# Kernel tuning notes

Measured on AMD Instinct MI355X. Metric: run time of the kernel, lower is better.

Reference implementation:

```python
import jax, jax.numpy as jnp
import numpy as np

B, S, H, E, D, K = 2, 2048, 2048, 8, 2048, 2


def setup_inputs() -> dict:
    key = jax.random.key(0)
    ks = jax.random.split(key, 4)
    # lecun_normal-style scaling: std = 1/sqrt(fan_in)
    return {
        "x": jax.random.normal(ks[0], (B, S, H), jnp.float32),
        "router_w": jax.random.normal(ks[1], (H, E), jnp.float32) / np.sqrt(H).astype(np.float32),
        "router_b": jnp.zeros((E,), jnp.float32),
        "expert_w": jax.random.normal(ks[2], (E, H, D), jnp.float32) / np.sqrt(H).astype(np.float32),
        "expert_b": jnp.zeros((E, D), jnp.float32),
        "out_w": jax.random.normal(ks[3], (D, D), jnp.float32) / np.sqrt(D).astype(np.float32),
        "out_b": jnp.zeros((D,), jnp.float32),
    }


def reference(x, router_w, router_b, expert_w, expert_b, out_w, out_b):
    num_experts = expert_w.shape[0]
    # Router: logits -> softmax -> top-2 -> renormalize
    router_logits = jnp.einsum("bsh,he->bse", x, router_w) + router_b
    router_probs = jax.nn.softmax(router_logits, axis=-1)
    top_k_probs, top_k_indices = jax.lax.top_k(router_probs, K)  # [B,S,K]
    top_k_probs = top_k_probs / jnp.sum(top_k_probs, axis=-1, keepdims=True)
    # Per-expert gate weight: sum of top-k probs routed to that expert. [B,S,E]
    onehot = jax.nn.one_hot(top_k_indices, num_experts, dtype=x.dtype)  # [B,S,K,E]
    gates = jnp.einsum("bsk,bske->bse", top_k_probs, onehot)
    # Dense per-expert GEMM + gelu (mask-and-multiply MoE; gate==0 kills unrouted tokens)
    expert_out = jax.nn.gelu(jnp.einsum("bsh,ehd->ebsd", x, expert_w) + expert_b[:, None, None, :])
    combined = jnp.einsum("bse,ebsd->bsd", gates, expert_out)
    # Output projection
    return jnp.einsum("bsd,df->bsf", combined, out_w) + out_b
```

## Files before the change

### kernel.cpp

```cpp
#include <hip/hip_runtime.h>
#include <stdint.h>

#define H_DIM 2048
#define E_NUM 8
#define D_DIM 2048
#define NTOK 4096
#define BM 128
#define BN 128
#define BK 32

typedef __bf16 bf16x8 __attribute__((ext_vector_type(8)));
typedef float f32x4 __attribute__((ext_vector_type(4)));

__device__ __forceinline__ unsigned short f2bf(float f) {
    union { float f; uint32_t u; } c; c.f = f;
    uint32_t r = (c.u + 0x7FFFu + ((c.u >> 16) & 1u)) >> 16;
    return (unsigned short)r;
}
__device__ __forceinline__ float bf2f(unsigned short h) {
    union { float f; uint32_t u; } c; c.u = ((uint32_t)h) << 16;
    return c.f;
}

__device__ __forceinline__ void gl_lds16(const unsigned short* g, unsigned short* l) {
    __builtin_amdgcn_global_load_lds(
        (const __attribute__((address_space(1))) unsigned int*)g,
        (__attribute__((address_space(3))) unsigned int*)l, 16, 0, 0);
}

__global__ __launch_bounds__(256) void router_cvt_kernel(
    const float* __restrict__ x, const float* __restrict__ rw,
    const float* __restrict__ rb, int* __restrict__ counts,
    uint32_t* __restrict__ tok, float* __restrict__ gate,
    unsigned short* __restrict__ xb) {
    int t = (blockIdx.x * 256 + threadIdx.x) >> 6;
    int lane = threadIdx.x & 63;
    const float* xr = x + (size_t)t * H_DIM;
    unsigned short* xo = xb + (size_t)t * H_DIM;
    float p[E_NUM];
#pragma unroll
    for (int e = 0; e < E_NUM; e++) p[e] = 0.f;
#pragma unroll
    for (int pass = 0; pass < H_DIM / 256; pass++) {
        int h = pass * 256 + lane * 4;
        float4 v = *(const float4*)(xr + h);
        ushort4 o;
        o.x = f2bf(v.x); o.y = f2bf(v.y); o.z = f2bf(v.z); o.w = f2bf(v.w);
        *(ushort4*)(xo + h) = o;
        const float* r0 = rw + (size_t)h * E_NUM;
#pragma unroll
        for (int e = 0; e < E_NUM; e++)
            p[e] += v.x * r0[e] + v.y * r0[e + 8] + v.z * r0[e + 16] + v.w * r0[e + 24];
    }
#pragma unroll
    for (int e = 0; e < E_NUM; e++) {
#pragma unroll
        for (int off = 1; off < 64; off <<= 1) p[e] += __shfl_xor(p[e], off, 64);
    }
    if (lane == 0) {
        float l[E_NUM];
#pragma unroll
        for (int e = 0; e < E_NUM; e++) l[e] = p[e] + rb[e];
        int e0 = 0;
#pragma unroll
        for (int e = 1; e < E_NUM; e++) if (l[e] > l[e0]) e0 = e;
        int e1 = (e0 == 0) ? 1 : 0;
#pragma unroll
        for (int e = 0; e < E_NUM; e++) if (e != e0 && l[e] > l[e1]) e1 = e;
        float g0 = 1.f / (1.f + __expf(l[e1] - l[e0]));
        float g1 = 1.f - g0;
        int p0 = atomicAdd(&counts[e0], 1);
        tok[e0 * NTOK + p0] = (uint32_t)t;
        gate[e0 * NTOK + p0] = g0;
        int p1 = atomicAdd(&counts[e1], 1);
        tok[e1 * NTOK + p1] = (uint32_t)t | (1u << 16);
        gate[e1 * NTOK + p1] = g1;
    }
}

__global__ __launch_bounds__(256) void transpose_cvt_kernel(
    const float* __restrict__ ew, const float* __restrict__ ow,
    unsigned short* __restrict__ ewT) {
    __shared__ unsigned short t[64][136];
    int z = blockIdx.z;
    const float* s = (z < 8) ? (ew + (size_t)z * H_DIM * D_DIM) : ow;
    unsigned short* d = ewT + (size_t)z * H_DIM * D_DIM;
    int n0 = blockIdx.x * 64, k0 = blockIdx.y * 128;
    int tid = threadIdx.x;
    int rr = tid >> 4;
    int c4 = (tid & 15) * 4;
#pragma unroll
    for (int p = 0; p < 8; p++) {
        int k = p * 16 + rr;
        float4 v = *(const float4*)(s + (size_t)(k0 + k) * D_DIM + n0 + c4);
        t[c4 + 0][k] = f2bf(v.x);
        t[c4 + 1][k] = f2bf(v.y);
        t[c4 + 2][k] = f2bf(v.z);
        t[c4 + 3][k] = f2bf(v.w);
    }
    __syncthreads();
    int kc = (tid & 15) * 8;
#pragma unroll
    for (int p = 0; p < 4; p++) {
        int n = p * 16 + rr;
        uint4 v = *(const uint4*)&t[n][kc];
        *(uint4*)(d + (size_t)(n0 + n) * H_DIM + k0 + kc) = v;
    }
}

__global__ __launch_bounds__(256) void expert_gemm_kernel(
    const unsigned short* __restrict__ xb,
    const unsigned short* __restrict__ ewT,
    const float* __restrict__ eb,
    const int* __restrict__ counts,
    const uint32_t* __restrict__ tok,
    const float* __restrict__ gate,
    unsigned short* __restrict__ Y)
{
    int e = blockIdx.z;
    int cnt = counts[e];
    int m0 = blockIdx.y * BM;
    if (m0 >= cnt) return;
    int n0 = blockIdx.x * BN;

    __shared__ unsigned short As[BM][BK];
    __shared__ unsigned short Bs[BN][BK];
    __shared__ uint32_t tok_s[BM];
    __shared__ float gate_s[BM];

    int tid = threadIdx.x;
    if (tid < BM) {
        int idx = m0 + tid;
        uint32_t tk = 0; float g = 0.f;
        if (idx < cnt) { tk = tok[e * NTOK + idx]; g = gate[e * NTOK + idx]; }
        tok_s[tid] = tk; gate_s[tid] = g;
    }
    __syncthreads();

    int lane = tid & 63;
    int wave = tid >> 6;
    int sr = lane >> 2;
    int sc = ((lane & 3) ^ ((lane >> 3) & 3)) * 8;
    int r0 = wave * 32 + sr;
    int r1 = wave * 32 + 16 + sr;
    const unsigned short* agp0 = xb + (size_t)(tok_s[r0] & 0xFFFFu) * H_DIM + sc;
    const unsigned short* agp1 = xb + (size_t)(tok_s[r1] & 0xFFFFu) * H_DIM + sc;
    const unsigned short* bbase = ewT + (size_t)e * D_DIM * H_DIM;
    const unsigned short* bgp0 = bbase + (size_t)(n0 + r0) * H_DIM + sc;
    const unsigned short* bgp1 = bbase + (size_t)(n0 + r1) * H_DIM + sc;
    unsigned short* la0 = &As[wave * 32][0];
    unsigned short* la1 = &As[wave * 32 + 16][0];
    unsigned short* lb0 = &Bs[wave * 32][0];
    unsigned short* lb1 = &Bs[wave * 32 + 16][0];

    int wm = (wave >> 1) * 64;
    int wn = (wave & 1) * 64;
    int row16 = lane & 15;
    int quad = lane >> 4;
    int slot = (quad ^ ((row16 >> 1) & 3)) * 16;
    int aoffA[4], aoffB[4];
#pragma unroll
    for (int i = 0; i < 4; i++) {
        aoffA[i] = (wm + i * 16 + row16) * (BK * 2) + slot;
        aoffB[i] = (wn + i * 16 + row16) * (BK * 2) + slot;
    }
    const char* pA = (const char*)&As[0][0];
    const char* pB = (const char*)&Bs[0][0];

    f32x4 acc[4][4];
#pragma unroll
    for (int i = 0; i < 4; i++)
#pragma unroll
        for (int j = 0; j < 4; j++) acc[i][j] = (f32x4)(0.f);

    for (int kk = 0; kk < H_DIM; kk += BK) {
        __syncthreads();
        gl_lds16(agp0 + kk, la0);
        gl_lds16(agp1 + kk, la1);
        gl_lds16(bgp0 + kk, lb0);
        gl_lds16(bgp1 + kk, lb1);
        __syncthreads();
        bf16x8 af[4], bff[4];
#pragma unroll
        for (int i = 0; i < 4; i++) {
            af[i] = *(const bf16x8*)(pA + aoffA[i]);
            bff[i] = *(const bf16x8*)(pB + aoffB[i]);
        }
#pragma unroll
        for (int i = 0; i < 4; i++)
#pragma unroll
            for (int j = 0; j < 4; j++)
                acc[i][j] = __builtin_amdgcn_mfma_f32_16x16x32_bf16(
                    af[i], bff[j], acc[i][j], 0, 0, 0);
    }

#pragma unroll
    for (int i = 0; i < 4; i++) {
        int rbase = wm + i * 16 + quad * 4;
#pragma unroll
        for (int j = 0; j < 4; j++) {
            int n = n0 + wn + j * 16 + row16;
            float bias = eb[e * D_DIM + n];
#pragma unroll
            for (int r = 0; r < 4; r++) {
                int lrow = rbase + r;
                if (m0 + lrow < cnt) {
                    uint32_t tk = tok_s[lrow];
                    float g = gate_s[lrow];
                    float v = acc[i][j][r] + bias;
                    float q = 0.7978845608028654f * (v + 0.044715f * v * v * v);
                    float gl = v / (1.f + __expf(-2.f * q));
                    int token = tk & 0xFFFF;
                    int slot2 = (tk >> 16) & 1;
                    Y[((size_t)token * 2 + slot2) * D_DIM + n] = f2bf(g * gl);
                }
            }
        }
    }
}

__global__ __launch_bounds__(256) void combine_kernel(
    const unsigned short* __restrict__ Y, unsigned short* __restrict__ comb) {
    int i = blockIdx.x * 256 + threadIdx.x;
    int t = i >> 8;
    int dc = (i & 255) * 8;
    uint4 u0 = *(const uint4*)(Y + (size_t)t * 2 * D_DIM + dc);
    uint4 u1 = *(const uint4*)(Y + ((size_t)t * 2 + 1) * D_DIM + dc);
    uint4 o;
    uint32_t* po = (uint32_t*)&o;
    const uint32_t* p0 = (const uint32_t*)&u0;
    const uint32_t* p1 = (const uint32_t*)&u1;
#pragma unroll
    for (int k = 0; k < 4; k++) {
        uint32_t a = p0[k], b = p1[k];
        float s0 = bf2f((unsigned short)(a & 0xFFFF)) + bf2f((unsigned short)(b & 0xFFFF));
        float s1 = bf2f((unsigned short)(a >> 16)) + bf2f((unsigned short)(b >> 16));
        po[k] = (uint32_t)f2bf(s0) | ((uint32_t)f2bf(s1) << 16);
    }
    *(uint4*)(comb + (size_t)t * D_DIM + dc) = o;
}

__global__ __launch_bounds__(256) void out_gemm_kernel(
    const unsigned short* __restrict__ comb,
    const unsigned short* __restrict__ owT,
    const float* __restrict__ ob,
    float* __restrict__ out) {
    int m0 = blockIdx.y * BM, n0 = blockIdx.x * BN;
    __shared__ unsigned short As[BM][BK];
    __shared__ unsigned short Bs[BN][BK];
    int tid = threadIdx.x;
    int lane = tid & 63;
    int wave = tid >> 6;
    int sr = lane >> 2;
    int sc = ((lane & 3) ^ ((lane >> 3) & 3)) * 8;
    int r0 = wave * 32 + sr;
    int r1 = wave * 32 + 16 + sr;
    const unsigned short* agp0 = comb + (size_t)(m0 + r0) * D_DIM + sc;
    const unsigned short* agp1 = comb + (size_t)(m0 + r1) * D_DIM + sc;
    const unsigned short* bgp0 = owT + (size_t)(n0 + r0) * D_DIM + sc;
    const unsigned short* bgp1 = owT + (size_t)(n0 + r1) * D_DIM + sc;
    unsigned short* la0 = &As[wave * 32][0];
    unsigned short* la1 = &As[wave * 32 + 16][0];
    unsigned short* lb0 = &Bs[wave * 32][0];
    unsigned short* lb1 = &Bs[wave * 32 + 16][0];

    int wm = (wave >> 1) * 64;
    int wn = (wave & 1) * 64;
    int row16 = lane & 15;
    int quad = lane >> 4;
    int slot = (quad ^ ((row16 >> 1) & 3)) * 16;
    int aoffA[4], aoffB[4];
#pragma unroll
    for (int i = 0; i < 4; i++) {
        aoffA[i] = (wm + i * 16 + row16) * (BK * 2) + slot;
        aoffB[i] = (wn + i * 16 + row16) * (BK * 2) + slot;
    }
    const char* pA = (const char*)&As[0][0];
    const char* pB = (const char*)&Bs[0][0];

    f32x4 acc[4][4];
#pragma unroll
    for (int i = 0; i < 4; i++)
#pragma unroll
        for (int j = 0; j < 4; j++) acc[i][j] = (f32x4)(0.f);

    for (int kk = 0; kk < D_DIM; kk += BK) {
        __syncthreads();
        gl_lds16(agp0 + kk, la0);
        gl_lds16(agp1 + kk, la1);
        gl_lds16(bgp0 + kk, lb0);
        gl_lds16(bgp1 + kk, lb1);
        __syncthreads();
        bf16x8 af[4], bff[4];
#pragma unroll
        for (int i = 0; i < 4; i++) {
            af[i] = *(const bf16x8*)(pA + aoffA[i]);
            bff[i] = *(const bf16x8*)(pB + aoffB[i]);
        }
#pragma unroll
        for (int i = 0; i < 4; i++)
#pragma unroll
            for (int j = 0; j < 4; j++)
                acc[i][j] = __builtin_amdgcn_mfma_f32_16x16x32_bf16(
                    af[i], bff[j], acc[i][j], 0, 0, 0);
    }

#pragma unroll
    for (int i = 0; i < 4; i++) {
        int rbase = m0 + wm + i * 16 + quad * 4;
#pragma unroll
        for (int j = 0; j < 4; j++) {
            int n = n0 + wn + j * 16 + row16;
            float bias = ob[n];
#pragma unroll
            for (int r = 0; r < 4; r++) {
                out[(size_t)(rbase + r) * D_DIM + n] = acc[i][j][r] + bias;
            }
        }
    }
}

extern "C" void kernel_launch(void* const* d_in, const int* in_sizes, int n_in,
                              void* d_out, int out_size, void* d_ws, size_t ws_size,
                              hipStream_t stream) {
    const float* x        = (const float*)d_in[0];
    const float* router_w = (const float*)d_in[1];
    const float* router_b = (const float*)d_in[2];
    const float* expert_w = (const float*)d_in[3];
    const float* expert_b = (const float*)d_in[4];
    const float* out_w    = (const float*)d_in[5];
    const float* out_b    = (const float*)d_in[6];
    float* out = (float*)d_out;

    char* w = (char*)d_ws;
    int* counts = (int*)w;
    uint32_t* tok = (uint32_t*)(w + 1024);
    float* gate = (float*)(w + 1024 + E_NUM * NTOK * 4);
    size_t off = 1024 + (size_t)2 * E_NUM * NTOK * 4;
    unsigned short* xb = (unsigned short*)(w + off);
    off += (size_t)NTOK * H_DIM * 2;
    unsigned short* ewT = (unsigned short*)(w + off);
    off += (size_t)E_NUM * H_DIM * D_DIM * 2;
    unsigned short* owT = (unsigned short*)(w + off);
    off += (size_t)D_DIM * D_DIM * 2;
    unsigned short* Y = (unsigned short*)(w + off);
    off += (size_t)NTOK * 2 * D_DIM * 2;
    unsigned short* comb = (unsigned short*)(w + off);

    hipMemsetAsync(d_ws, 0, 1024, stream);
    router_cvt_kernel<<<NTOK / 4, 256, 0, stream>>>(x, router_w, router_b,
                                                    counts, tok, gate, xb);
    transpose_cvt_kernel<<<dim3(32, 16, 9), 256, 0, stream>>>(expert_w, out_w, ewT);
    expert_gemm_kernel<<<dim3(16, 32, 8), 256, 0, stream>>>(
        xb, ewT, expert_b, counts, tok, gate, Y);
    combine_kernel<<<NTOK * D_DIM / 8 / 256, 256, 0, stream>>>(Y, comb);
    out_gemm_kernel<<<dim3(16, 32), 256, 0, stream>>>(comb, owT, out_b, out);
}
```

Measured before the change: 529.2 us.

## Double-buffer LDS tiles in both GEMMs and compact expert tile grid

Result: slower. 550.8 us (+4.1%).

```diff
diff --git a/kernel.cpp b/kernel.cpp
--- a/kernel.cpp
+++ b/kernel.cpp
@@ -8,6 +8,8 @@
 #define BM 128
 #define BN 128
 #define BK 32
+#define MAXTILES 72
+#define BUFB (BM * BK * 2)
 
 typedef __bf16 bf16x8 __attribute__((ext_vector_type(8)));
 typedef float f32x4 __attribute__((ext_vector_type(4)));
@@ -26,6 +28,23 @@
     __builtin_amdgcn_global_load_lds(
         (const __attribute__((address_space(1))) unsigned int*)g,
         (__attribute__((address_space(3))) unsigned int*)l, 16, 0, 0);
+}
+
+__device__ __forceinline__ void mfma_step(const char* pA, const char* pB,
+                                          const int* aoffA, const int* aoffB,
+                                          f32x4 (&acc)[4][4]) {
+    bf16x8 af[4], bf_[4];
+#pragma unroll
+    for (int i = 0; i < 4; i++) {
+        af[i] = *(const bf16x8*)(pA + aoffA[i]);
+        bf_[i] = *(const bf16x8*)(pB + aoffB[i]);
+    }
+#pragma unroll
+    for (int i = 0; i < 4; i++)
+#pragma unroll
+        for (int j = 0; j < 4; j++)
+            acc[i][j] = __builtin_amdgcn_mfma_f32_16x16x32_bf16(
+                af[i], bf_[j], acc[i][j], 0, 0, 0);
 }
 
 __global__ __launch_bounds__(256) void router_cvt_kernel(
@@ -75,6 +94,19 @@
         int p1 = atomicAdd(&counts[e1], 1);
         tok[e1 * NTOK + p1] = (uint32_t)t | (1u << 16);
         gate[e1 * NTOK + p1] = g1;
+    }
+}
+
+__global__ void build_tiles_kernel(const int* __restrict__ counts,
+                                   int* __restrict__ ntiles,
+                                   int2* __restrict__ tab) {
+    if (threadIdx.x == 0 && blockIdx.x == 0) {
+        int off = 0;
+        for (int e = 0; e < E_NUM; e++) {
+            int c = counts[e];
+            for (int m0 = 0; m0 < c; m0 += BM) tab[off++] = make_int2(e, m0);
+        }
+        *ntiles = off;
     }
 }
 
@@ -113,18 +145,20 @@
     const unsigned short* __restrict__ ewT,
     const float* __restrict__ eb,
     const int* __restrict__ counts,
+    const int* __restrict__ ntiles,
+    const int2* __restrict__ tab,
     const uint32_t* __restrict__ tok,
     const float* __restrict__ gate,
     unsigned short* __restrict__ Y)
 {
-    int e = blockIdx.z;
+    if ((int)blockIdx.y >= *ntiles) return;
+    int2 te = tab[blockIdx.y];
+    int e = te.x, m0 = te.y;
     int cnt = counts[e];
-    int m0 = blockIdx.y * BM;
-    if (m0 >= cnt) return;
     int n0 = blockIdx.x * BN;
 
-    __shared__ unsigned short As[BM][BK];
-    __shared__ unsigned short Bs[BN][BK];
+    __shared__ unsigned short As[2][BM][BK];
+    __shared__ unsigned short Bs[2][BN][BK];
     __shared__ uint32_t tok_s[BM];
     __shared__ float gate_s[BM];
 
@@ -148,10 +182,6 @@
     const unsigned short* bbase = ewT + (size_t)e * D_DIM * H_DIM;
     const unsigned short* bgp0 = bbase + (size_t)(n0 + r0) * H_DIM + sc;
     const unsigned short* bgp1 = bbase + (size_t)(n0 + r1) * H_DIM + sc;
-    unsigned short* la0 = &As[wave * 32][0];
-    unsigned short* la1 = &As[wave * 32 + 16][0];
-    unsigned short* lb0 = &Bs[wave * 32][0];
-    unsigned short* lb1 = &Bs[wave * 32 + 16][0];
 
     int wm = (wave >> 1) * 64;
     int wn = (wave & 1) * 64;
@@ -164,8 +194,16 @@
         aoffA[i] = (wm + i * 16 + row16) * (BK * 2) + slot;
         aoffB[i] = (wn + i * 16 + row16) * (BK * 2) + slot;
     }
-    const char* pA = (const char*)&As[0][0];
-    const char* pB = (const char*)&Bs[0][0];
+    const char* pA0 = (const char*)&As[0][0][0];
+    const char* pB0 = (const char*)&Bs[0][0][0];
+    const char* pA1 = pA0 + BUFB;
+    const char* pB1 = pB0 + BUFB;
+
+#define EPREF(kn, b)                                          \
+    gl_lds16(agp0 + (kn), &As[b][wave * 32][0]);              \
+    gl_lds16(agp1 + (kn), &As[b][wave * 32 + 16][0]);         \
+    gl_lds16(bgp0 + (kn), &Bs[b][wave * 32][0]);              \
+    gl_lds16(bgp1 + (kn), &Bs[b][wave * 32 + 16][0]);
 
     f32x4 acc[4][4];
 #pragma unroll
@@ -173,26 +211,16 @@
 #pragma unroll
         for (int j = 0; j < 4; j++) acc[i][j] = (f32x4)(0.f);
 
-    for (int kk = 0; kk < H_DIM; kk += BK) {
+    EPREF(0, 0);
+    for (int kk = 0; kk < H_DIM; kk += 2 * BK) {
         __syncthreads();
-        gl_lds16(agp0 + kk, la0);
-        gl_lds16(agp1 + kk, la1);
-        gl_lds16(bgp0 + kk, lb0);
-        gl_lds16(bgp1 + kk, lb1);
+        EPREF(kk + BK, 1);
+        mfma_step(pA0, pB0, aoffA, aoffB, acc);
         __syncthreads();
-        bf16x8 af[4], bff[4];
-#pragma unroll
-        for (int i = 0; i < 4; i++) {
-            af[i] = *(const bf16x8*)(pA + aoffA[i]);
-            bff[i] = *(const bf16x8*)(pB + aoffB[i]);
-        }
-#pragma unroll
-        for (int i = 0; i < 4; i++)
-#pragma unroll
-            for (int j = 0; j < 4; j++)
-                acc[i][j] = __builtin_amdgcn_mfma_f32_16x16x32_bf16(
-                    af[i], bff[j], acc[i][j], 0, 0, 0);
-    }
+        if (kk + 2 * BK < H_DIM) { EPREF(kk + 2 * BK, 0); }
+        mfma_step(pA1, pB1, aoffA, aoffB, acc);
+    }
+#undef EPREF
 
 #pragma unroll
     for (int i = 0; i < 4; i++) {
@@ -246,8 +274,8 @@
     const float* __restrict__ ob,
     float* __restrict__ out) {
     int m0 = blockIdx.y * BM, n0 = blockIdx.x * BN;
-    __shared__ unsigned short As[BM][BK];
-    __shared__ unsigned short Bs[BN][BK];
+    __shared__ unsigned short As[2][BM][BK];
+    __shared__ unsigned short Bs[2][BN][BK];
     int tid = threadIdx.x;
     int lane = tid & 63;
     int wave = tid >> 6;
@@ -259,10 +287,6 @@
     const unsigned short* agp1 = comb + (size_t)(m0 + r1) * D_DIM + sc;
     const unsigned short* bgp0 = owT + (size_t)(n0 + r0) * D_DIM + sc;
     const unsigned short* bgp1 = owT + (size_t)(n0 + r1) * D_DIM + sc;
-    unsigned short* la0 = &As[wave * 32][0];
-    unsigned short* la1 = &As[wave * 32 + 16][0];
-    unsigned short* lb0 = &Bs[wave * 32][0];
-    unsigned short* lb1 = &Bs[wave * 32 + 16][0];
 
     int wm = (wave >> 1) * 64;
     int wn = (wave & 1) * 64;
@@ -275,8 +299,16 @@
         aoffA[i] = (wm + i * 16 + row16) * (BK * 2) + slot;
         aoffB[i] = (wn + i * 16 + row16) * (BK * 2) + slot;
     }
-    const char* pA = (const char*)&As[0][0];
-    const char* pB = (const char*)&Bs[0][0];
+    const char* pA0 = (const char*)&As[0][0][0];
+    const char* pB0 = (const char*)&Bs[0][0][0];
+    const char* pA1 = pA0 + BUFB;
+    const char* pB1 = pB0 + BUFB;
+
+#define OPREF(kn, b)                                          \
+    gl_lds16(agp0 + (kn), &As[b][wave * 32][0]);              \
+    gl_lds16(agp1 + (kn), &As[b][wave * 32 + 16][0]);         \
+    gl_lds16(bgp0 + (kn), &Bs[b][wave * 32][0]);              \
+    gl_lds16(bgp1 + (kn), &Bs[b][wave * 32 + 16][0]);
 
     f32x4 acc[4][4];
 #pragma unroll
@@ -284,26 +316,16 @@
 #pragma unroll
         for (int j = 0; j < 4; j++) acc[i][j] = (f32x4)(0.f);
 
-    for (int kk = 0; kk < D_DIM; kk += BK) {
+    OPREF(0, 0);
+    for (int kk = 0; kk < D_DIM; kk += 2 * BK) {
         __syncthreads();
-        gl_lds16(agp0 + kk, la0);
-        gl_lds16(agp1 + kk, la1);
-        gl_lds16(bgp0 + kk, lb0);
-        gl_lds16(bgp1 + kk, lb1);
+        OPREF(kk + BK, 1);
+        mfma_step(pA0, pB0, aoffA, aoffB, acc);
         __syncthreads();
-        bf16x8 af[4], bff[4];
-#pragma unroll
-        for (int i = 0; i < 4; i++) {
-            af[i] = *(const bf16x8*)(pA + aoffA[i]);
-            bff[i] = *(const bf16x8*)(pB + aoffB[i]);
-        }
-#pragma unroll
-        for (int i = 0; i < 4; i++)
-#pragma unroll
-            for (int j = 0; j < 4; j++)
-                acc[i][j] = __builtin_amdgcn_mfma_f32_16x16x32_bf16(
-                    af[i], bff[j], acc[i][j], 0, 0, 0);
-    }
+        if (kk + 2 * BK < D_DIM) { OPREF(kk + 2 * BK, 0); }
+        mfma_step(pA1, pB1, aoffA, aoffB, acc);
+    }
+#undef OPREF
 
 #pragma unroll
     for (int i = 0; i < 4; i++) {
@@ -334,6 +356,8 @@
 
     char* w = (char*)d_ws;
     int* counts = (int*)w;
+    int* ntiles = (int*)(w + 64);
+    int2* tab = (int2*)(w + 128);
     uint32_t* tok = (uint32_t*)(w + 1024);
     float* gate = (float*)(w + 1024 + E_NUM * NTOK * 4);
     size_t off = 1024 + (size_t)2 * E_NUM * NTOK * 4;
@@ -350,9 +374,10 @@
     hipMemsetAsync(d_ws, 0, 1024, stream);
     router_cvt_kernel<<<NTOK / 4, 256, 0, stream>>>(x, router_w, router_b,
                                                     counts, tok, gate, xb);
+    build_tiles_kernel<<<1, 64, 0, stream>>>(counts, ntiles, tab);
     transpose_cvt_kernel<<<dim3(32, 16, 9), 256, 0, stream>>>(expert_w, out_w, ewT);
-    expert_gemm_kernel<<<dim3(16, 32, 8), 256, 0, stream>>>(
-        xb, ewT, expert_b, counts, tok, gate, Y);
+    expert_gemm_kernel<<<dim3(16, MAXTILES), 256, 0, stream>>>(
+        xb, ewT, expert_b, counts, ntiles, tab, tok, gate, Y);
     combine_kernel<<<NTOK * D_DIM / 8 / 256, 256, 0, stream>>>(Y, comb);
     out_gemm_kernel<<<dim3(16, 32), 256, 0, stream>>>(comb, owT, out_b, out);
 }
```

## Fuse top-2 combine into output GEMM A-tile load and shrink M tile

Applied to the files above, without the earlier changes.

Result: slower. 553.2 us (+4.5%).

```diff
diff --git a/kernel.cpp b/kernel.cpp
--- a/kernel.cpp
+++ b/kernel.cpp
@@ -219,86 +219,77 @@
     }
 }
 
-__global__ __launch_bounds__(256) void combine_kernel(
-    const unsigned short* __restrict__ Y, unsigned short* __restrict__ comb) {
-    int i = blockIdx.x * 256 + threadIdx.x;
-    int t = i >> 8;
-    int dc = (i & 255) * 8;
-    uint4 u0 = *(const uint4*)(Y + (size_t)t * 2 * D_DIM + dc);
-    uint4 u1 = *(const uint4*)(Y + ((size_t)t * 2 + 1) * D_DIM + dc);
-    uint4 o;
-    uint32_t* po = (uint32_t*)&o;
-    const uint32_t* p0 = (const uint32_t*)&u0;
-    const uint32_t* p1 = (const uint32_t*)&u1;
-#pragma unroll
-    for (int k = 0; k < 4; k++) {
-        uint32_t a = p0[k], b = p1[k];
-        float s0 = bf2f((unsigned short)(a & 0xFFFF)) + bf2f((unsigned short)(b & 0xFFFF));
-        float s1 = bf2f((unsigned short)(a >> 16)) + bf2f((unsigned short)(b >> 16));
-        po[k] = (uint32_t)f2bf(s0) | ((uint32_t)f2bf(s1) << 16);
-    }
-    *(uint4*)(comb + (size_t)t * D_DIM + dc) = o;
-}
-
+#define OBM 64
 __global__ __launch_bounds__(256) void out_gemm_kernel(
-    const unsigned short* __restrict__ comb,
+    const unsigned short* __restrict__ Y,
     const unsigned short* __restrict__ owT,
     const float* __restrict__ ob,
     float* __restrict__ out) {
-    int m0 = blockIdx.y * BM, n0 = blockIdx.x * BN;
-    __shared__ unsigned short As[BM][BK];
+    int m0 = blockIdx.y * OBM, n0 = blockIdx.x * BN;
+    __shared__ unsigned short As[OBM][BK];
     __shared__ unsigned short Bs[BN][BK];
     int tid = threadIdx.x;
     int lane = tid & 63;
     int wave = tid >> 6;
+
+    int arow = tid >> 2;
+    int achunk = tid & 3;
+    const unsigned short* y0 = Y + (size_t)(m0 + arow) * 2 * D_DIM + achunk * 8;
+    const unsigned short* y1 = y0 + D_DIM;
+    unsigned short* adst = &As[arow][(achunk ^ ((arow >> 1) & 3)) * 8];
+
     int sr = lane >> 2;
     int sc = ((lane & 3) ^ ((lane >> 3) & 3)) * 8;
     int r0 = wave * 32 + sr;
     int r1 = wave * 32 + 16 + sr;
-    const unsigned short* agp0 = comb + (size_t)(m0 + r0) * D_DIM + sc;
-    const unsigned short* agp1 = comb + (size_t)(m0 + r1) * D_DIM + sc;
     const unsigned short* bgp0 = owT + (size_t)(n0 + r0) * D_DIM + sc;
     const unsigned short* bgp1 = owT + (size_t)(n0 + r1) * D_DIM + sc;
-    unsigned short* la0 = &As[wave * 32][0];
-    unsigned short* la1 = &As[wave * 32 + 16][0];
     unsigned short* lb0 = &Bs[wave * 32][0];
     unsigned short* lb1 = &Bs[wave * 32 + 16][0];
 
-    int wm = (wave >> 1) * 64;
+    int wm = (wave >> 1) * 32;
     int wn = (wave & 1) * 64;
     int row16 = lane & 15;
     int quad = lane >> 4;
     int slot = (quad ^ ((row16 >> 1) & 3)) * 16;
-    int aoffA[4], aoffB[4];
-#pragma unroll
-    for (int i = 0; i < 4; i++) {
+    int aoffA[2], aoffB[4];
+#pragma unroll
+    for (int i = 0; i < 2; i++)
         aoffA[i] = (wm + i * 16 + row16) * (BK * 2) + slot;
-        aoffB[i] = (wn + i * 16 + row16) * (BK * 2) + slot;
-    }
+#pragma unroll
+    for (int j = 0; j < 4; j++)
+        aoffB[j] = (wn + j * 16 + row16) * (BK * 2) + slot;
     const char* pA = (const char*)&As[0][0];
     const char* pB = (const char*)&Bs[0][0];
 
-    f32x4 acc[4][4];
-#pragma unroll
-    for (int i = 0; i < 4; i++)
+    f32x4 acc[2][4];
+#pragma unroll
+    for (int i = 0; i < 2; i++)
 #pragma unroll
         for (int j = 0; j < 4; j++) acc[i][j] = (f32x4)(0.f);
 
     for (int kk = 0; kk < D_DIM; kk += BK) {
+        bf16x8 a0 = *(const bf16x8*)(y0 + kk);
+        bf16x8 a1 = *(const bf16x8*)(y1 + kk);
+        unsigned short sum[8];
+#pragma unroll
+        for (int q = 0; q < 8; q++) {
+            union { __bf16 b; unsigned short u; } u0, u1;
+            u0.b = a0[q]; u1.b = a1[q];
+            sum[q] = f2bf(bf2f(u0.u) + bf2f(u1.u));
+        }
         __syncthreads();
-        gl_lds16(agp0 + kk, la0);
-        gl_lds16(agp1 + kk, la1);
+        *(uint4*)adst = *(const uint4*)sum;
         gl_lds16(bgp0 + kk, lb0);
         gl_lds16(bgp1 + kk, lb1);
         __syncthreads();
-        bf16x8 af[4], bff[4];
-#pragma unroll
-        for (int i = 0; i < 4; i++) {
-            af[i] = *(const bf16x8*)(pA + aoffA[i]);
-            bff[i] = *(const bf16x8*)(pB + aoffB[i]);
-        }
-#pragma unroll
-        for (int i = 0; i < 4; i++)
+        bf16x8 af[2], bff[4];
+#pragma unroll
+        for (int i = 0; i < 2; i++) af[i] = *(const bf16x8*)(pA + aoffA[i]);
+#pragma unroll
+        for (int j = 0; j < 4; j++) bff[j] = *(const bf16x8*)(pB + aoffB[j]);
+#pragma unroll
+        for (int i = 0; i < 2; i++)
 #pragma unroll
             for (int j = 0; j < 4; j++)
                 acc[i][j] = __builtin_amdgcn_mfma_f32_16x16x32_bf16(
@@ -306,7 +297,7 @@
     }
 
 #pragma unroll
-    for (int i = 0; i < 4; i++) {
+    for (int i = 0; i < 2; i++) {
         int rbase = m0 + wm + i * 16 + quad * 4;
 #pragma unroll
         for (int j = 0; j < 4; j++) {
@@ -344,8 +335,6 @@
     unsigned short* owT = (unsigned short*)(w + off);
     off += (size_t)D_DIM * D_DIM * 2;
     unsigned short* Y = (unsigned short*)(w + off);
-    off += (size_t)NTOK * 2 * D_DIM * 2;
-    unsigned short* comb = (unsigned short*)(w + off);
 
     hipMemsetAsync(d_ws, 0, 1024, stream);
     router_cvt_kernel<<<NTOK / 4, 256, 0, stream>>>(x, router_w, router_b,
@@ -353,6 +342,5 @@
     transpose_cvt_kernel<<<dim3(32, 16, 9), 256, 0, stream>>>(expert_w, out_w, ewT);
     expert_gemm_kernel<<<dim3(16, 32, 8), 256, 0, stream>>>(
         xb, ewT, expert_b, counts, tok, gate, Y);
-    combine_kernel<<<NTOK * D_DIM / 8 / 256, 256, 0, stream>>>(Y, comb);
-    out_gemm_kernel<<<dim3(16, 32), 256, 0, stream>>>(comb, owT, out_b, out);
-}
+    out_gemm_kernel<<<dim3(16, NTOK / OBM), 256, 0, stream>>>(Y, owT, out_b, out);
+}
```

## Compact expert tiles into a table and fuse combine into output GEMM

Applied to the files above, without the earlier changes.

After: 557.7 us. +5.4%, slower.

```diff
diff --git a/kernel.cpp b/kernel.cpp
--- a/kernel.cpp
+++ b/kernel.cpp
@@ -8,6 +8,7 @@
 #define BM 128
 #define BN 128
 #define BK 32
+#define MAXTILES 72
 
 typedef __bf16 bf16x8 __attribute__((ext_vector_type(8)));
 typedef float f32x4 __attribute__((ext_vector_type(4)));
@@ -75,6 +76,19 @@
         int p1 = atomicAdd(&counts[e1], 1);
         tok[e1 * NTOK + p1] = (uint32_t)t | (1u << 16);
         gate[e1 * NTOK + p1] = g1;
+    }
+}
+
+__global__ void build_tiles_kernel(const int* __restrict__ counts,
+                                   int* __restrict__ ntiles,
+                                   int2* __restrict__ tab) {
+    if (threadIdx.x == 0 && blockIdx.x == 0) {
+        int off = 0;
+        for (int e = 0; e < E_NUM; e++) {
+            int c = counts[e];
+            for (int m0 = 0; m0 < c; m0 += BM) tab[off++] = make_int2(e, m0);
+        }
+        *ntiles = off;
     }
 }
 
@@ -113,14 +127,16 @@
     const unsigned short* __restrict__ ewT,
     const float* __restrict__ eb,
     const int* __restrict__ counts,
+    const int* __restrict__ ntiles,
+    const int2* __restrict__ tab,
     const uint32_t* __restrict__ tok,
     const float* __restrict__ gate,
     unsigned short* __restrict__ Y)
 {
-    int e = blockIdx.z;
+    if ((int)blockIdx.y >= *ntiles) return;
+    int2 te = tab[blockIdx.y];
+    int e = te.x, m0 = te.y;
     int cnt = counts[e];
-    int m0 = blockIdx.y * BM;
-    if (m0 >= cnt) return;
     int n0 = blockIdx.x * BN;
 
     __shared__ unsigned short As[BM][BK];
@@ -219,29 +235,8 @@
     }
 }
 
-__global__ __launch_bounds__(256) void combine_kernel(
-    const unsigned short* __restrict__ Y, unsigned short* __restrict__ comb) {
-    int i = blockIdx.x * 256 + threadIdx.x;
-    int t = i >> 8;
-    int dc = (i & 255) * 8;
-    uint4 u0 = *(const uint4*)(Y + (size_t)t * 2 * D_DIM + dc);
-    uint4 u1 = *(const uint4*)(Y + ((size_t)t * 2 + 1) * D_DIM + dc);
-    uint4 o;
-    uint32_t* po = (uint32_t*)&o;
-    const uint32_t* p0 = (const uint32_t*)&u0;
-    const uint32_t* p1 = (const uint32_t*)&u1;
-#pragma unroll
-    for (int k = 0; k < 4; k++) {
-        uint32_t a = p0[k], b = p1[k];
-        float s0 = bf2f((unsigned short)(a & 0xFFFF)) + bf2f((unsigned short)(b & 0xFFFF));
-        float s1 = bf2f((unsigned short)(a >> 16)) + bf2f((unsigned short)(b >> 16));
-        po[k] = (uint32_t)f2bf(s0) | ((uint32_t)f2bf(s1) << 16);
-    }
-    *(uint4*)(comb + (size_t)t * D_DIM + dc) = o;
-}
-
 __global__ __launch_bounds__(256) void out_gemm_kernel(
-    const unsigned short* __restrict__ comb,
+    const unsigned short* __restrict__ Y,
     const unsigned short* __restrict__ owT,
     const float* __restrict__ ob,
     float* __restrict__ out) {
@@ -251,16 +246,23 @@
     int tid = threadIdx.x;
     int lane = tid & 63;
     int wave = tid >> 6;
+
+    int arow = tid >> 2;
+    int achunk = tid & 3;
+    int aslot = (achunk ^ ((arow >> 1) & 3)) * 8;
+    const unsigned short* ya0 = Y + (size_t)(m0 + arow) * 2 * D_DIM + achunk * 8;
+    const unsigned short* ya1 = ya0 + D_DIM;
+    const unsigned short* yb0 = Y + (size_t)(m0 + arow + 64) * 2 * D_DIM + achunk * 8;
+    const unsigned short* yb1 = yb0 + D_DIM;
+    unsigned short* adst0 = &As[arow][aslot];
+    unsigned short* adst1 = &As[arow + 64][aslot];
+
     int sr = lane >> 2;
     int sc = ((lane & 3) ^ ((lane >> 3) & 3)) * 8;
     int r0 = wave * 32 + sr;
     int r1 = wave * 32 + 16 + sr;
-    const unsigned short* agp0 = comb + (size_t)(m0 + r0) * D_DIM + sc;
-    const unsigned short* agp1 = comb + (size_t)(m0 + r1) * D_DIM + sc;
     const unsigned short* bgp0 = owT + (size_t)(n0 + r0) * D_DIM + sc;
     const unsigned short* bgp1 = owT + (size_t)(n0 + r1) * D_DIM + sc;
-    unsigned short* la0 = &As[wave * 32][0];
-    unsigned short* la1 = &As[wave * 32 + 16][0];
     unsigned short* lb0 = &Bs[wave * 32][0];
     unsigned short* lb1 = &Bs[wave * 32 + 16][0];
 
@@ -285,9 +287,21 @@
         for (int j = 0; j < 4; j++) acc[i][j] = (f32x4)(0.f);
 
     for (int kk = 0; kk < D_DIM; kk += BK) {
+        bf16x8 a0 = *(const bf16x8*)(ya0 + kk);
+        bf16x8 a1 = *(const bf16x8*)(ya1 + kk);
+        bf16x8 b0 = *(const bf16x8*)(yb0 + kk);
+        bf16x8 b1 = *(const bf16x8*)(yb1 + kk);
+        unsigned short s0[8], s1[8];
+#pragma unroll
+        for (int q = 0; q < 8; q++) {
+            union { __bf16 b; unsigned short u; } x0, x1, z0, z1;
+            x0.b = a0[q]; x1.b = a1[q]; z0.b = b0[q]; z1.b = b1[q];
+            s0[q] = f2bf(bf2f(x0.u) + bf2f(x1.u));
+            s1[q] = f2bf(bf2f(z0.u) + bf2f(z1.u));
+        }
         __syncthreads();
-        gl_lds16(agp0 + kk, la0);
-        gl_lds16(agp1 + kk, la1);
+        *(uint4*)adst0 = *(const uint4*)s0;
+        *(uint4*)adst1 = *(const uint4*)s1;
         gl_lds16(bgp0 + kk, lb0);
         gl_lds16(bgp1 + kk, lb1);
         __syncthreads();
@@ -334,6 +348,8 @@
 
     char* w = (char*)d_ws;
     int* counts = (int*)w;
+    int* ntiles = (int*)(w + 64);
+    int2* tab = (int2*)(w + 128);
     uint32_t* tok = (uint32_t*)(w + 1024);
     float* gate = (float*)(w + 1024 + E_NUM * NTOK * 4);
     size_t off = 1024 + (size_t)2 * E_NUM * NTOK * 4;
@@ -344,15 +360,13 @@
     unsigned short* owT = (unsigned short*)(w + off);
     off += (size_t)D_DIM * D_DIM * 2;
     unsigned short* Y = (unsigned short*)(w + off);
-    off += (size_t)NTOK * 2 * D_DIM * 2;
-    unsigned short* comb = (unsigned short*)(w + off);
 
     hipMemsetAsync(d_ws, 0, 1024, stream);
     router_cvt_kernel<<<NTOK / 4, 256, 0, stream>>>(x, router_w, router_b,
                                                     counts, tok, gate, xb);
+    build_tiles_kernel<<<1, 64, 0, stream>>>(counts, ntiles, tab);
     transpose_cvt_kernel<<<dim3(32, 16, 9), 256, 0, stream>>>(expert_w, out_w, ewT);
-    expert_gemm_kernel<<<dim3(16, 32, 8), 256, 0, stream>>>(
-        xb, ewT, expert_b, counts, tok, gate, Y);
-    combine_kernel<<<NTOK * D_DIM / 8 / 256, 256, 0, stream>>>(Y, comb);
-    out_gemm_kernel<<<dim3(16, 32), 256, 0, stream>>>(comb, owT, out_b, out);
-}
+    expert_gemm_kernel<<<dim3(16, MAXTILES), 256, 0, stream>>>(
+        xb, ewT, expert_b, counts, ntiles, tab, tok, gate, Y);
+    out_gemm_kernel<<<dim3(16, NTOK / BM), 256, 0, stream>>>(Y, owT, out_b, out);
+}
```
